# Kernel tuning notes

Measured on AMD Instinct MI355X. Metric: run time of the kernel, lower is better.

Reference implementation:

```python
import jax, jax.numpy as jnp
import numpy as np

B, C, H, W = 8, 32, 512, 512
BN_EPS = 1e-5


def setup_inputs() -> dict:
    key = jax.random.key(0)
    k1, k2, k3, k4 = jax.random.split(key, 4)
    x = jax.random.normal(k1, (B, C, H, W), dtype=jnp.float32)
    # 1x1 conv weight: [out=4, in=4*C] (kaiming-like scale)
    w_compress = jax.random.normal(k2, (4, 4 * C), dtype=jnp.float32) / np.sqrt(4 * C)
    gamma = jnp.ones((4,), dtype=jnp.float32)
    beta = jnp.zeros((4,), dtype=jnp.float32)
    return {"x": x, "w_compress": w_compress, "gamma": gamma, "beta": beta}


def _four_dir(x):
    # zero-pad H and W by 1; shifted view at (di, dj) gives x[i+di, j+dj]
    xp = jnp.pad(x, ((0, 0), (0, 0), (1, 1), (1, 1)))

    def sh(di, dj):
        return jax.lax.dynamic_slice(xp, (0, 0, 1 + di, 1 + dj), x.shape)

    # PyTorch conv = cross-correlation: kernel one at (r,c) reads x[i+r-1, j+c-1]
    ne = sh(-1, +1) - x
    nw = sh(-1, -1) - x
    se = sh(+1, +1) - x
    sw = sh(+1, -1) - x
    return jnp.concatenate([ne, nw, se, sw], axis=1)  # [B, 4C, H, W]


def reference(x, w_compress, gamma, beta):
    feat = _four_dir(x)
    # 1x1 conv: channel mixing 4C -> 4
    y = jnp.einsum("oc,bchw->bohw", w_compress, feat)
    # BatchNorm2d (training mode: batch statistics, biased variance)
    mean = jnp.mean(y, axis=(0, 2, 3), keepdims=True)
    var = jnp.var(y, axis=(0, 2, 3), keepdims=True)
    y_hat = (y - mean) * jax.lax.rsqrt(var + BN_EPS)
    return y_hat * gamma[None, :, None, None] + beta[None, :, None, None]
```

## Files before the change

### kernel.cpp

```cpp
#include <hip/hip_runtime.h>

#define B_ 8
#define C_ 32
#define H_ 512
#define W_ 512
#define HW_ (H_ * W_)
#define BN_EPS 1e-5f

typedef float f4v __attribute__((ext_vector_type(4)));


__global__ __launch_bounds__(256, 2) void fourdir_compute(
    const float* __restrict__ x,
    const float* __restrict__ w,
    float* __restrict__ y,
    float* __restrict__ sums)
{
    __shared__ f4v wl4[5][C_];
    const int t = threadIdx.x;
    {
        float* wl = (float*)wl4;
        for (int idx = t; idx < 4 * 4 * C_; idx += 256) {
            int o  = idx & 3;
            int dc = idx >> 2;
            wl[idx] = w[o * (4 * C_) + dc];
        }
    }
    __syncthreads();
    if (t < 4 * C_) {
        float* wl = (float*)wl4;
        wl[512 + t] = -(wl[t] + wl[128 + t] + wl[256 + t] + wl[384 + t]);
    }
    __syncthreads();

    const int lane = t & 63;
    const int wv   = t >> 6;
    const int cg   = lane & 15;
    const int sr   = lane >> 4;
    const int j0 = (blockIdx.x << 6) + (cg << 2);
    const int i0 = (blockIdx.y << 6) + (wv << 4) + (sr << 2);
    const int b  = blockIdx.z;
    const float* xb = x + (size_t)b * C_ * HW_;

    const bool jm = (j0 > 0);
    const bool jp = (j0 + 4 < W_);
    const bool tv = (i0 > 0);
    const bool bv = (i0 + 4 < H_);

    int off[6];
    {
        const int rows[6] = { tv ? i0 - 1 : 0, i0, i0 + 1, i0 + 2, i0 + 3,
                              bv ? i0 + 4 : H_ - 1 };
#pragma unroll
        for (int k = 0; k < 6; ++k) off[k] = rows[k] * W_ + j0;
    }

    f4v acc[4][4];
#pragma unroll
    for (int p = 0; p < 4; ++p)
#pragma unroll
        for (int q = 0; q < 4; ++q) acc[p][q] = f4v{0.f, 0.f, 0.f, 0.f};

#pragma unroll 2
    for (int c = 0; c < C_; ++c) {
        const float* xc = xb + (size_t)c * HW_;
        f4v  vr[6];
        float lf[6], rt[6];
#pragma unroll
        for (int k = 0; k < 6; ++k) {
            vr[k] = *(const f4v*)(xc + off[k]);
            lf[k] = jm ? xc[off[k] - 1] : 0.f;
            rt[k] = jp ? xc[off[k] + 4] : 0.f;
        }
        if (!tv) { vr[0] = f4v{0.f,0.f,0.f,0.f}; lf[0] = 0.f; rt[0] = 0.f; }
        if (!bv) { vr[5] = f4v{0.f,0.f,0.f,0.f}; lf[5] = 0.f; rt[5] = 0.f; }

        const f4v wne = wl4[0][c];
        const f4v wnw = wl4[1][c];
        const f4v wse = wl4[2][c];
        const f4v wsw = wl4[3][c];
        const f4v wct = wl4[4][c];

#pragma unroll
        for (int p = 0; p < 4; ++p) {
#pragma unroll
            for (int q = 0; q < 4; ++q) {
                const float ne = (q < 3) ? vr[p][q + 1]     : rt[p];
                const float nw = (q > 0) ? vr[p][q - 1]     : lf[p];
                const float se = (q < 3) ? vr[p + 2][q + 1] : rt[p + 2];
                const float sw = (q > 0) ? vr[p + 2][q - 1] : lf[p + 2];
                const float ct = vr[p + 1][q];
                acc[p][q] += wne * ne + wnw * nw + wse * se + wsw * sw + wct * ct;
            }
        }
    }

#pragma unroll
    for (int p = 0; p < 4; ++p) {
        const size_t base = (size_t)(i0 + p) * W_ + j0;
#pragma unroll
        for (int o = 0; o < 4; ++o) {
            f4v st = { acc[p][0][o], acc[p][1][o], acc[p][2][o], acc[p][3][o] };
            *(f4v*)(y + ((size_t)(b * 4 + o)) * HW_ + base) = st;
        }
    }

    f4v s0 = f4v{0.f,0.f,0.f,0.f}, s1 = f4v{0.f,0.f,0.f,0.f};
#pragma unroll
    for (int p = 0; p < 4; ++p)
#pragma unroll
        for (int q = 0; q < 4; ++q) {
            s0 += acc[p][q];
            s1 += acc[p][q] * acc[p][q];
        }

    float vals[8] = { s0[0], s0[1], s0[2], s0[3], s1[0], s1[1], s1[2], s1[3] };
#pragma unroll
    for (int k = 0; k < 8; ++k) {
        float v = vals[k];
#pragma unroll
        for (int o = 32; o >= 1; o >>= 1) v += __shfl_xor(v, o, 64);
        vals[k] = v;
    }

    __shared__ float red[4][8];
    if (lane == 0) {
#pragma unroll
        for (int k = 0; k < 8; ++k) red[wv][k] = vals[k];
    }
    __syncthreads();
    if (t < 8) {
        const float s = red[0][t] + red[1][t] + red[2][t] + red[3][t];
        atomicAdd(&sums[t], s);
    }
}

__global__ __launch_bounds__(256) void bn_norm(
    float* __restrict__ y,
    const float* __restrict__ sums,
    const float* __restrict__ gamma,
    const float* __restrict__ beta)
{
    const int gid = blockIdx.x * 256 + threadIdx.x;
    const size_t base = (size_t)gid * 4;
    const int o = (int)((base / HW_) & 3);

    const float n = (float)((size_t)B_ * HW_);
    const float mean  = sums[o] / n;
    const float var   = sums[4 + o] / n - mean * mean;
    const float scale = rsqrtf(var + BN_EPS) * gamma[o];
    const float shift = beta[o] - mean * scale;

    float4 v = *(const float4*)(y + base);
    v.x = v.x * scale + shift;
    v.y = v.y * scale + shift;
    v.z = v.z * scale + shift;
    v.w = v.w * scale + shift;
    *(float4*)(y + base) = v;
}

extern "C" void kernel_launch(void* const* d_in, const int* in_sizes, int n_in,
                              void* d_out, int out_size, void* d_ws, size_t ws_size,
                              hipStream_t stream) {
    const float* x     = (const float*)d_in[0];
    const float* w     = (const float*)d_in[1];
    const float* gamma = (const float*)d_in[2];
    const float* beta  = (const float*)d_in[3];
    float* out  = (float*)d_out;
    float* sums = (float*)d_ws;

    hipMemsetAsync(sums, 0, 8 * sizeof(float), stream);

    dim3 gridA(W_ / 64, H_ / 64, B_);
    fourdir_compute<<<gridA, 256, 0, stream>>>(x, w, out, sums);

    const int nf4 = (B_ * 4 * HW_) / 4;
    bn_norm<<<nf4 / 256, 256, 0, stream>>>(out, sums, gamma, beta);
}
```

Baseline: 396.0 us.

## Retile to wave-wide rows, share halo via shuffles, double-buffer channel loads

Result: no change. 391.0 us (-1.3%).

```diff
diff --git a/kernel.cpp b/kernel.cpp
--- a/kernel.cpp
+++ b/kernel.cpp
@@ -35,24 +35,25 @@
 
     const int lane = t & 63;
     const int wv   = t >> 6;
-    const int cg   = lane & 15;
-    const int sr   = lane >> 4;
-    const int j0 = (blockIdx.x << 6) + (cg << 2);
-    const int i0 = (blockIdx.y << 6) + (wv << 4) + (sr << 2);
+    const int c0 = blockIdx.x << 8;
+    const int i0 = (blockIdx.y << 4) + (wv << 2);
     const int b  = blockIdx.z;
+    const int j  = c0 + (lane << 2);
     const float* xb = x + (size_t)b * C_ * HW_;
 
-    const bool jm = (j0 > 0);
-    const bool jp = (j0 + 4 < W_);
+    const bool jm = (c0 > 0);
+    const bool jp = (c0 + 256 < W_);
     const bool tv = (i0 > 0);
     const bool bv = (i0 + 4 < H_);
+    const bool edgeL = (lane == 0);
+    const bool edgeR = (lane == 63);
 
     int off[6];
     {
         const int rows[6] = { tv ? i0 - 1 : 0, i0, i0 + 1, i0 + 2, i0 + 3,
-                              bv ? i0 + 4 : H_ - 1 };
-#pragma unroll
-        for (int k = 0; k < 6; ++k) off[k] = rows[k] * W_ + j0;
+                              bv ? i0 + 4 : 0 };
+#pragma unroll
+        for (int k = 0; k < 6; ++k) off[k] = rows[k] * W_ + j;
     }
 
     f4v acc[4][4];
@@ -61,25 +62,38 @@
 #pragma unroll
         for (int q = 0; q < 4; ++q) acc[p][q] = f4v{0.f, 0.f, 0.f, 0.f};
 
-#pragma unroll 2
-    for (int c = 0; c < C_; ++c) {
+    auto LOADCH = [&](int c, f4v (&vr)[6], float (&le)[6], float (&re)[6]) {
         const float* xc = xb + (size_t)c * HW_;
-        f4v  vr[6];
-        float lf[6], rt[6];
+#pragma unroll
+        for (int k = 0; k < 6; ++k) vr[k] = *(const f4v*)(xc + off[k]);
 #pragma unroll
         for (int k = 0; k < 6; ++k) {
-            vr[k] = *(const f4v*)(xc + off[k]);
-            lf[k] = jm ? xc[off[k] - 1] : 0.f;
-            rt[k] = jp ? xc[off[k] + 4] : 0.f;
-        }
-        if (!tv) { vr[0] = f4v{0.f,0.f,0.f,0.f}; lf[0] = 0.f; rt[0] = 0.f; }
-        if (!bv) { vr[5] = f4v{0.f,0.f,0.f,0.f}; lf[5] = 0.f; rt[5] = 0.f; }
-
+            float l = 0.f, r = 0.f;
+            if (edgeL && jm) l = xc[off[k] - 1];
+            if (edgeR && jp) r = xc[off[k] + 4];
+            le[k] = l;
+            re[k] = r;
+        }
+        if (!tv) { vr[0] = f4v{0.f,0.f,0.f,0.f}; le[0] = 0.f; re[0] = 0.f; }
+        if (!bv) { vr[5] = f4v{0.f,0.f,0.f,0.f}; le[5] = 0.f; re[5] = 0.f; }
+    };
+
+    auto COMPCH = [&](int c, const f4v (&vr)[6],
+                      const float (&le)[6], const float (&re)[6]) {
         const f4v wne = wl4[0][c];
         const f4v wnw = wl4[1][c];
         const f4v wse = wl4[2][c];
         const f4v wsw = wl4[3][c];
         const f4v wct = wl4[4][c];
+
+        float lf[6], rt[6];
+#pragma unroll
+        for (int k = 0; k < 6; ++k) {
+            const float l = __shfl_up(vr[k][3], 1, 64);
+            const float r = __shfl_down(vr[k][0], 1, 64);
+            lf[k] = edgeL ? le[k] : l;
+            rt[k] = edgeR ? re[k] : r;
+        }
 
 #pragma unroll
         for (int p = 0; p < 4; ++p) {
@@ -93,11 +107,26 @@
                 acc[p][q] += wne * ne + wnw * nw + wse * se + wsw * sw + wct * ct;
             }
         }
-    }
+    };
+
+    f4v vrA[6], vrB[6];
+    float leA[6], reA[6], leB[6], reB[6];
+
+    LOADCH(0, vrA, leA, reA);
+#pragma unroll 1
+    for (int cc = 0; cc < C_ - 2; cc += 2) {
+        LOADCH(cc + 1, vrB, leB, reB);
+        COMPCH(cc, vrA, leA, reA);
+        LOADCH(cc + 2, vrA, leA, reA);
+        COMPCH(cc + 1, vrB, leB, reB);
+    }
+    LOADCH(C_ - 1, vrB, leB, reB);
+    COMPCH(C_ - 2, vrA, leA, reA);
+    COMPCH(C_ - 1, vrB, leB, reB);
 
 #pragma unroll
     for (int p = 0; p < 4; ++p) {
-        const size_t base = (size_t)(i0 + p) * W_ + j0;
+        const size_t base = (size_t)(i0 + p) * W_ + j;
 #pragma unroll
         for (int o = 0; o < 4; ++o) {
             f4v st = { acc[p][0][o], acc[p][1][o], acc[p][2][o], acc[p][3][o] };
@@ -171,7 +200,7 @@
 
     hipMemsetAsync(sums, 0, 8 * sizeof(float), stream);
 
-    dim3 gridA(W_ / 64, H_ / 64, B_);
+    dim3 gridA(W_ / 256, H_ / 16, B_);
     fourdir_compute<<<gridA, 256, 0, stream>>>(x, w, out, sums);
 
     const int nf4 = (B_ * 4 * HW_) / 4;
```
